# Performance work log

Hardware: AMD Instinct MI355X
Metric: run time of the kernel (lower is better)

## Reference

```python
import jax, jax.numpy as jnp
import numpy as np

B, L, D = 4, 4096, 768
K, Kq, NREP, H, M = 12, 6, 2, 64, 1
KSZ = 4
DIM_MEM = K * H                 # 768
DIM_MEMT = DIM_MEM + K          # 780
DIM_Q = Kq * H * M * 2          # 768
DIM_CONV = DIM_MEMT + DIM_Q     # 1548
DIM_SKIP = D // 4               # 192
DIM_SWH = H * 3 * 2             # 384 (dim_swiglu_head)
DIM_SW = K * DIM_SWH            # 4608
DIM_TOTAL = DIM_CONV + DIM_SKIP + K  # 1752
FLAT = K * H * M                # 768


def _rms(x, w, eps=1e-6):
    return x * jax.lax.rsqrt(jnp.mean(x * x, axis=-1, keepdims=True) + eps) * w


def _dwconv_causal(x, w):
    # depthwise causal conv: x (B,L,C), w (KSZ,C); left-pad KSZ-1
    pad = jnp.pad(x, ((0, 0), (KSZ - 1, 0), (0, 0)))
    Lx = x.shape[1]
    return sum(pad[:, j:j + Lx, :] * w[j] for j in range(KSZ))


def _forward(x, W_in, conv_w, wk, wq, theta_raw, w_int_raw, dt_scale, dt_bias,
             log_A, phase_scale, W_gate, gn_weight, W_readout, W_skip, W_out):
    Bx, Lx, _ = x.shape
    z_all = x @ W_in
    z_conv = z_all[..., :DIM_CONV]
    c_skip = z_all[..., DIM_CONV:DIM_CONV + DIM_SKIP]
    gate_logits = z_all[..., DIM_CONV + DIM_SKIP:]
    z_conv = jax.nn.silu(_dwconv_causal(z_conv, conv_w))
    z_mem = z_conv[..., :DIM_MEMT]
    q_raw = z_conv[..., DIM_MEMT:]
    k_val = _rms(z_mem[..., :DIM_MEM].reshape(Bx, Lx, K, H), wk)
    s_raw = z_mem[..., DIM_MEM:]                       # (B,L,K)
    q = _rms(q_raw, wq).reshape(Bx, Lx, Kq, 1, H, M, 2)
    q_re, q_im = q[..., 0], q[..., 1]
    # M==1 path: theta from logit-parameterized grid, w_int = exp(clipped raw)
    theta = 0.001 + (3.0 - 0.001) * jax.nn.sigmoid(theta_raw)   # (1,1,K,H,1)
    w_int = jnp.exp(jnp.clip(w_int_raw, -5.0, 5.0))             # (1,1,Kq,NREP,H,1)
    dt = jnp.clip(jax.nn.softplus(jnp.clip(dt_scale * s_raw + dt_bias, -20.0, 20.0)), 0.001, 0.1)
    A_disc = jnp.clip(-jnp.exp(log_A) * dt, -20.0, 0.0)         # (B,L,K)
    kf = k_val[..., None]                                       # (B,L,K,H,1)
    ks = kf * phase_scale[None, None, :, None, None]
    phi = ks / (1.0 + jnp.abs(ks)) * theta
    kvw = kf * dt[..., None, None]
    re = kvw * jnp.cos(phi)
    im = kvw * jnp.sin(phi)
    stack = jnp.concatenate([re.reshape(Bx, Lx, FLAT), im.reshape(Bx, Lx, FLAT)], axis=-1)
    decay = jnp.repeat(jnp.exp(A_disc), H * M, axis=-1)
    decay = jnp.concatenate([decay, decay], axis=-1)            # (B,L,2*FLAT)

    def step(carry, inp):
        xt, dc = inp
        s = dc * carry + xt
        return s, s

    init = jnp.zeros((Bx, 2 * FLAT), stack.dtype)
    _, acc = jax.lax.scan(step, init, (stack.transpose(1, 0, 2), decay.transpose(1, 0, 2)))
    acc = acc.transpose(1, 0, 2)                                # (B,L,2*FLAT)
    re_acc = acc[..., :FLAT].reshape(Bx, Lx, Kq, NREP, H, M)
    im_acc = acc[..., FLAT:].reshape(Bx, Lx, Kq, NREP, H, M)
    match_re = re_acc * q_re + im_acc * q_im
    match_im = im_acc * q_re - re_acc * q_im
    out_re = jnp.sum(match_re * w_int, axis=-1).reshape(Bx, Lx, K, H)
    out_im = jnp.sum(match_im * w_int, axis=-1).reshape(Bx, Lx, K, H)
    oc = jnp.concatenate([out_re, out_im], axis=-1).reshape(Bx, Lx, K * 2 * H)
    # GatedRMSNorm: x*sigmoid(gate) -> rmsnorm -> *weight
    g = oc * jax.nn.sigmoid(gate_logits @ W_gate)
    oc_n = _rms(g, gn_weight)
    y_spec = jnp.einsum('blkf,kfn->blkn', oc_n.reshape(Bx, Lx, K, 2 * H), W_readout)
    y_skip = (c_skip @ W_skip).reshape(Bx, Lx, K, DIM_SWH)
    val, gate2 = jnp.split(y_spec + y_skip, 2, axis=-1)
    y = val * jax.nn.silu(gate2)                                # (B,L,K,3H)
    return y.reshape(Bx, Lx, -1) @ W_out                        # (B,L,D)


def setup_inputs() -> dict:
    key = jax.random.key(0)
    ks = jax.random.split(key, 8)
    # theta_raw init: logit of normalized geomspace grid (M==1 branch)
    grid = np.geomspace(0.001, 3.0, K).reshape(1, 1, K, 1, 1)
    base = np.tile(grid, (1, 1, 1, H, 1))
    u = np.clip((base - 0.001) / (3.0 - 0.001), 1e-4, 1 - 1e-4)
    theta_raw = jnp.asarray(np.log(u) - np.log(1 - u), jnp.float32)
    return {
        'x': jax.random.normal(ks[0], (B, L, D), jnp.float32),
        'W_in': jax.random.normal(ks[1], (D, DIM_TOTAL), jnp.float32) * 0.02,
        'conv_w': jax.random.normal(ks[2], (KSZ, DIM_CONV), jnp.float32) * 0.2,
        'wk': jnp.ones((H,), jnp.float32),
        'wq': jnp.ones((DIM_Q,), jnp.float32),
        'theta_raw': theta_raw,
        'w_int_raw': jnp.zeros((1, 1, Kq, NREP, H, M), jnp.float32),
        'dt_scale': jnp.ones((K,), jnp.float32),
        'dt_bias': jnp.asarray(np.log(np.expm1(np.geomspace(0.001, 0.1, K))), jnp.float32),
        'log_A': jnp.asarray(np.log(np.geomspace(1.0, 16.0, K)), jnp.float32),
        'phase_scale': jnp.ones((K,), jnp.float32),
        'W_gate': jax.random.normal(ks[3], (K, K * 2 * H), jnp.float32) * 0.1,
        'gn_weight': jnp.ones((K * 2 * H,), jnp.float32),
        'W_readout': jax.random.normal(ks[4], (K, 2 * H, DIM_SWH), jnp.float32) * float(np.sqrt(2.0 / (2 * H + DIM_SWH))),
        'W_skip': jax.random.normal(ks[5], (DIM_SKIP, DIM_SW), jnp.float32) * 0.02,
        'W_out': jax.random.normal(ks[6], (K * 3 * H, D), jnp.float32) * 0.02,
    }


def reference(x, W_in, conv_w, wk, wq, theta_raw, w_int_raw, dt_scale, dt_bias,
              log_A, phase_scale, W_gate, gn_weight, W_readout, W_skip, W_out):
    return _forward(x, W_in, conv_w, wk, wq, theta_raw, w_int_raw, dt_scale, dt_bias,
                    log_A, phase_scale, W_gate, gn_weight, W_readout, W_skip, W_out)
```

## Files before the change

kernel.cpp:

```cpp
#include <hip/hip_runtime.h>
#include <hip/hip_bf16.h>
#include <cstdint>
#include <cstddef>

#define BB 4
#define LL 4096
#define DD 768
#define KK 12
#define HH 64
#define KSZ 4
#define DIM_MEM 768
#define DIM_MEMT 780
#define DIM_Q 768
#define DIM_CONV 1548
#define DIM_SKIP 192
#define DIM_SWH 384
#define DIM_TOTAL 1752
#define TTOK (BB*LL)
#define NCHUNK 128
#define LCHUNK 32
#define N1REAL 1752
#define N1PAD 1792
#define DGATE (KK*2*HH)

typedef unsigned short ushort_t;
typedef __attribute__((ext_vector_type(8))) short short8v;
typedef __attribute__((ext_vector_type(4))) float f32x4;

__device__ __forceinline__ float sigm(float x) {
    return __builtin_amdgcn_rcpf(1.0f + __expf(-x));
}
__device__ __forceinline__ float softplus_fast(float x) {
    return (x > 0.f) ? (x + __logf(1.0f + __expf(-x))) : __logf(1.0f + __expf(x));
}
__device__ __forceinline__ ushort_t f2bf(float f) {
    __hip_bfloat16 h = __float2bfloat16(f);
    return __builtin_bit_cast(ushort_t, h);
}
__device__ __forceinline__ float bf2f(ushort_t u) {
    const uint32_t i = ((uint32_t)u) << 16;
    return __builtin_bit_cast(float, i);
}
__device__ __forceinline__ float blockReduceSum256(float v, float* sbuf) {
    #pragma unroll
    for (int off = 32; off > 0; off >>= 1) v += __shfl_xor(v, off);
    const int wid = threadIdx.x >> 6;
    __syncthreads();
    if ((threadIdx.x & 63) == 0) sbuf[wid] = v;
    __syncthreads();
    return sbuf[0] + sbuf[1] + sbuf[2] + sbuf[3];
}
__device__ __forceinline__ void gload_lds16(const void* g, void* l) {
    __builtin_amdgcn_global_load_lds(
        (const __attribute__((address_space(1))) void*)g,
        (__attribute__((address_space(3))) void*)l, 16, 0, 0);
}

__launch_bounds__(256)
__global__ void cast_bf16(const float* __restrict__ in, ushort_t* __restrict__ out, int n4) {
    const int stride = gridDim.x * 256;
    for (int i = blockIdx.x * 256 + threadIdx.x; i < n4; i += stride) {
        const float4 v = reinterpret_cast<const float4*>(in)[i];
        ushort4 o;
        o.x = f2bf(v.x); o.y = f2bf(v.y); o.z = f2bf(v.z); o.w = f2bf(v.w);
        reinterpret_cast<ushort4*>(out)[i] = o;
    }
}

__global__ void transpose_cast(const float* __restrict__ in, ushort_t* __restrict__ out,
                               int R, int Cc, int Cpad) {
    __shared__ float tile[32][33];
    const int tx = threadIdx.x, ty = threadIdx.y;
    const int c0 = blockIdx.x * 32, r0 = blockIdx.y * 32;
    #pragma unroll
    for (int rr = ty; rr < 32; rr += 8) {
        const int r = r0 + rr, c = c0 + tx;
        tile[rr][tx] = (r < R && c < Cc) ? in[(size_t)r * Cc + c] : 0.f;
    }
    __syncthreads();
    #pragma unroll
    for (int rr = ty; rr < 32; rr += 8) {
        const int c = c0 + rr, r = r0 + tx;
        if (c < Cpad && r < R)
            out[(size_t)c * R + r] = f2bf(tile[tx][rr]);
    }
}

__global__ void prep_bt(const float* __restrict__ Wr, const float* __restrict__ Wskip,
                        ushort_t* __restrict__ Btv, ushort_t* __restrict__ Btg) {
    const int k = blockIdx.x, n = blockIdx.y, kk = threadIdx.x;
    float v, g;
    if (kk < 128) {
        const size_t base = ((size_t)k * 128 + kk) * DIM_SWH;
        v = Wr[base + n];
        g = Wr[base + 192 + n];
    } else {
        const size_t base = (size_t)(kk - 128) * (KK * DIM_SWH) + (size_t)k * DIM_SWH;
        v = Wskip[base + n];
        g = Wskip[base + 192 + n];
    }
    const size_t o = ((size_t)k * 192 + n) * 320 + kk;
    Btv[o] = f2bf(v);
    Btg[o] = f2bf(g);
}

__global__ void prep_wint(const float* __restrict__ w_int_raw, float* __restrict__ wint) {
    const int i = blockIdx.x * 256 + threadIdx.x;
    if (i < KK * HH) {
        float wr = w_int_raw[i];
        wr = fminf(fmaxf(wr, -5.f), 5.f);
        wint[i] = expf(wr);
    }
}

template <bool BF16OUT>
__launch_bounds__(256)
__global__ void mfma_gemm(const ushort_t* __restrict__ A, const ushort_t* __restrict__ Bt,
                          void* __restrict__ Cv, int Nreal, int K) {
    __shared__ ushort_t As[2][128 * 32];
    __shared__ ushort_t Bs[2][128 * 32];
    const int tid = threadIdx.x;
    const int lane = tid & 63, w = tid >> 6;
    const int m0 = blockIdx.x * 128, n0 = blockIdx.y * 128;
    const int wm = w & 1, wn = w >> 1;
    const int nkt = K >> 5;
    const int lrow = lane >> 2;
    const int lcol = (lane & 3) * 8;

    f32x4 acc[4][4] = {};

    auto stage = [&](int buf, int k0) {
        #pragma unroll
        for (int i = 0; i < 2; ++i) {
            const int seg = w * 2 + i;
            const int row = seg * 16 + lrow;
            gload_lds16(&A[(size_t)(m0 + row) * K + k0 + lcol], &As[buf][seg * 512]);
            gload_lds16(&Bt[(size_t)(n0 + row) * K + k0 + lcol], &Bs[buf][seg * 512]);
        }
    };

    stage(0, 0);
    for (int kt = 0; kt < nkt; ++kt) {
        const int cur = kt & 1;
        __syncthreads();
        if (kt + 1 < nkt) stage(cur ^ 1, (kt + 1) << 5);
        short8v a[4], b[4];
        #pragma unroll
        for (int i = 0; i < 4; ++i)
            a[i] = *(const short8v*)&As[cur][(wm * 64 + i * 16 + (lane & 15)) * 32 + (lane >> 4) * 8];
        #pragma unroll
        for (int j = 0; j < 4; ++j)
            b[j] = *(const short8v*)&Bs[cur][(wn * 64 + j * 16 + (lane & 15)) * 32 + (lane >> 4) * 8];
        #pragma unroll
        for (int i = 0; i < 4; ++i)
            #pragma unroll
            for (int j = 0; j < 4; ++j)
                acc[i][j] = __builtin_amdgcn_mfma_f32_16x16x32_bf16(a[i], b[j], acc[i][j], 0, 0, 0);
    }
    #pragma unroll
    for (int i = 0; i < 4; ++i) {
        const int rbase = m0 + wm * 64 + i * 16 + (lane >> 4) * 4;
        #pragma unroll
        for (int j = 0; j < 4; ++j) {
            const int col = n0 + wn * 64 + j * 16 + (lane & 15);
            if (col < Nreal) {
                #pragma unroll
                for (int r = 0; r < 4; ++r) {
                    if constexpr (BF16OUT)
                        ((ushort_t*)Cv)[(size_t)(rbase + r) * Nreal + col] = f2bf(acc[i][j][r]);
                    else
                        ((float*)Cv)[(size_t)(rbase + r) * Nreal + col] = acc[i][j][r];
                }
            }
        }
    }
}

__launch_bounds__(256)
__global__ void gemm2_mfma(const ushort_t* __restrict__ OCNb, const ushort_t* __restrict__ CskB,
                           const ushort_t* __restrict__ Btv, const ushort_t* __restrict__ Btg,
                           ushort_t* __restrict__ Y) {
    __shared__ ushort_t As[2][128 * 64];
    __shared__ ushort_t Bvs[2][64 * 64];
    __shared__ ushort_t Bgs[2][64 * 64];
    const int tid = threadIdx.x;
    const int lane = tid & 63, w = tid >> 6;
    const int m0 = blockIdx.x * 128;
    const int n0 = blockIdx.y * 64;
    const int k  = blockIdx.z;
    const int wm = w & 1, wn = w >> 1;
    const int lrow = lane >> 3;
    const int lcol = (lane & 7) * 8;
    const ushort_t* btv = Btv + (size_t)k * 192 * 320;
    const ushort_t* btg = Btg + (size_t)k * 192 * 320;

    f32x4 accV[4][2] = {};
    f32x4 accG[4][2] = {};

    auto stage = [&](int buf, int kt) {
        #pragma unroll
        for (int i = 0; i < 4; ++i) {
            const int seg = w * 4 + i;
            const int row = seg * 8 + lrow;
            const ushort_t* src = (kt < 2)
                ? OCNb + (size_t)(m0 + row) * DGATE + k * 128 + kt * 64 + lcol
                : CskB + (size_t)(m0 + row) * DIM_SKIP + (kt - 2) * 64 + lcol;
            gload_lds16(src, &As[buf][seg * 512]);
        }
        #pragma unroll
        for (int i = 0; i < 2; ++i) {
            const int seg = w * 2 + i;
            const int row = seg * 8 + lrow;
            gload_lds16(btv + (size_t)(n0 + row) * 320 + kt * 64 + lcol, &Bvs[buf][seg * 512]);
            gload_lds16(btg + (size_t)(n0 + row) * 320 + kt * 64 + lcol, &Bgs[buf][seg * 512]);
        }
    };

    stage(0, 0);
    for (int kt = 0; kt < 5; ++kt) {
        const int cur = kt & 1;
        __syncthreads();
        if (kt + 1 < 5) stage(cur ^ 1, kt + 1);
        #pragma unroll
        for (int kk = 0; kk < 2; ++kk) {
            short8v a[4], bv[2], bg[2];
            #pragma unroll
            for (int i = 0; i < 4; ++i)
                a[i] = *(const short8v*)&As[cur][(wm * 64 + i * 16 + (lane & 15)) * 64 + kk * 32 + (lane >> 4) * 8];
            #pragma unroll
            for (int j = 0; j < 2; ++j) {
                bv[j] = *(const short8v*)&Bvs[cur][(wn * 32 + j * 16 + (lane & 15)) * 64 + kk * 32 + (lane >> 4) * 8];
                bg[j] = *(const short8v*)&Bgs[cur][(wn * 32 + j * 16 + (lane & 15)) * 64 + kk * 32 + (lane >> 4) * 8];
            }
            #pragma unroll
            for (int i = 0; i < 4; ++i)
                #pragma unroll
                for (int j = 0; j < 2; ++j) {
                    accV[i][j] = __builtin_amdgcn_mfma_f32_16x16x32_bf16(a[i], bv[j], accV[i][j], 0, 0, 0);
                    accG[i][j] = __builtin_amdgcn_mfma_f32_16x16x32_bf16(a[i], bg[j], accG[i][j], 0, 0, 0);
                }
        }
    }
    #pragma unroll
    for (int i = 0; i < 4; ++i) {
        const int rbase = m0 + wm * 64 + i * 16 + (lane >> 4) * 4;
        #pragma unroll
        for (int j = 0; j < 2; ++j) {
            const int col = k * 192 + n0 + wn * 32 + j * 16 + (lane & 15);
            #pragma unroll
            for (int r = 0; r < 4; ++r) {
                const float g = accG[i][j][r];
                Y[(size_t)(rbase + r) * (KK * 3 * HH) + col] = f2bf(accV[i][j][r] * (g * sigm(g)));
            }
        }
    }
}

__launch_bounds__(64)
__global__ void feat_scan(const ushort_t* __restrict__ Zb, const float* __restrict__ conv_w,
                          const float* __restrict__ wk, const float* __restrict__ theta_raw,
                          const float* __restrict__ dt_scale, const float* __restrict__ dt_bias,
                          const float* __restrict__ log_A, const float* __restrict__ phase_scale,
                          float2* __restrict__ acc, float* __restrict__ pcum,
                          float2* __restrict__ cend, float* __restrict__ cp) {
    const int blk = blockIdx.x;
    const int bk = blk / NCHUNK, chunk = blk - bk * NCHUNK;
    const int b = bk / KK, k = bk - b * KK;
    const int h = threadIdx.x;
    const int t0 = chunk * LCHUNK;
    const int cm_ch = k * HH + h;
    const int cs_ch = DIM_MEM + k;

    const float w0 = conv_w[0 * DIM_CONV + cm_ch];
    const float w1 = conv_w[1 * DIM_CONV + cm_ch];
    const float w2 = conv_w[2 * DIM_CONV + cm_ch];
    const float w3 = conv_w[3 * DIM_CONV + cm_ch];
    const float s0 = conv_w[0 * DIM_CONV + cs_ch];
    const float s1 = conv_w[1 * DIM_CONV + cs_ch];
    const float s2 = conv_w[2 * DIM_CONV + cs_ch];
    const float s3 = conv_w[3 * DIM_CONV + cs_ch];
    const float wkh = wk[h];
    const float th = 0.001f + (3.0f - 0.001f) * sigm(theta_raw[cm_ch]);
    const float ps = phase_scale[k];
    const float dts = dt_scale[k], dtb = dt_bias[k];
    const float eA = expf(log_A[k]);

    const size_t rowb = (size_t)b * LL;
    auto zm_at = [&](int t) -> float {
        return (t >= 0) ? bf2f(Zb[(rowb + t) * DIM_TOTAL + cm_ch]) : 0.f;
    };
    auto zs_at = [&](int t) -> float {
        return (t >= 0) ? bf2f(Zb[(rowb + t) * DIM_TOTAL + cs_ch]) : 0.f;
    };
    float zm3 = zm_at(t0 - 3), zm2 = zm_at(t0 - 2), zm1 = zm_at(t0 - 1);
    float zs3 = zs_at(t0 - 3), zs2 = zs_at(t0 - 2), zs1 = zs_at(t0 - 1);

    float are = 0.f, aim = 0.f, P = 1.f;
    #pragma unroll 4
    for (int tt = 0; tt < LCHUNK; ++tt) {
        const int t = t0 + tt;
        const float zm0 = bf2f(Zb[(rowb + t) * DIM_TOTAL + cm_ch]);
        const float zs0 = bf2f(Zb[(rowb + t) * DIM_TOTAL + cs_ch]);
        float cm = fmaf(w0, zm3, fmaf(w1, zm2, fmaf(w2, zm1, w3 * zm0)));
        float cs = fmaf(s0, zs3, fmaf(s1, zs2, fmaf(s2, zs1, s3 * zs0)));
        const float um = cm * sigm(cm);
        const float us = cs * sigm(cs);
        float ssq = um * um;
        #pragma unroll
        for (int off = 32; off > 0; off >>= 1) ssq += __shfl_xor(ssq, off);
        const float kval = um * rsqrtf(ssq * (1.0f / (float)HH) + 1e-6f) * wkh;
        float lin = fminf(fmaxf(fmaf(dts, us, dtb), -20.f), 20.f);
        float dt = fminf(fmaxf(softplus_fast(lin), 0.001f), 0.1f);
        const float Ad = fminf(fmaxf(-eA * dt, -20.f), 0.f);
        const float dec = __expf(Ad);
        const float ks = kval * ps;
        const float phi = ks / (1.0f + fabsf(ks)) * th;
        const float kvw = kval * dt;
        float sp, cq;
        __sincosf(phi, &sp, &cq);
        are = fmaf(dec, are, kvw * cq);
        aim = fmaf(dec, aim, kvw * sp);
        P *= dec;
        acc[((size_t)bk * LL + t) * HH + h] = make_float2(are, aim);
        if (h == 0) pcum[(size_t)bk * LL + t] = P;
        zm3 = zm2; zm2 = zm1; zm1 = zm0;
        zs3 = zs2; zs2 = zs1; zs1 = zs0;
    }
    cend[(size_t)blk * HH + h] = make_float2(are, aim);
    if (h == 0) cp[blk] = P;
}

__launch_bounds__(128)
__global__ void scan_b(const float* __restrict__ cend, const float* __restrict__ cp,
                       float* __restrict__ carry) {
    const int bk = blockIdx.x;
    const int c = threadIdx.x;
    float cur = 0.f;
    for (int ch = 0; ch < NCHUNK; ++ch) {
        const size_t idx = (size_t)bk * NCHUNK + ch;
        carry[idx * 128 + c] = cur;
        cur = fmaf(cp[idx], cur, cend[idx * 128 + c]);
    }
}

__launch_bounds__(256)
__global__ void combine_kernel(const float2* __restrict__ acc, const float* __restrict__ pcum,
                               const float2* __restrict__ carry, const ushort_t* __restrict__ Zb,
                               const float* __restrict__ conv_w, const float* __restrict__ wq,
                               const float* __restrict__ wintG, const float* __restrict__ W_gate,
                               const float* __restrict__ gn_weight,
                               ushort_t* __restrict__ ocnB, ushort_t* __restrict__ cskB) {
    __shared__ float q_sh[DIM_Q];
    __shared__ float g_sh[DGATE];
    __shared__ float gl[KK];
    __shared__ float red[8];
    const int tok = blockIdx.x;
    const int b = tok / LL, t = tok % LL;
    const int tid = threadIdx.x;
    const int chunk = t / LCHUNK;
    const size_t zrow = (size_t)tok * DIM_TOTAL;

    if (tid < KK) gl[tid] = bf2f(Zb[zrow + DIM_CONV + DIM_SKIP + tid]);
    if (tid < DIM_SKIP) cskB[(size_t)tok * DIM_SKIP + tid] = Zb[zrow + DIM_CONV + tid];

    float part = 0.f;
    float qv[3];
    #pragma unroll
    for (int it = 0; it < 3; ++it) {
        const int c = tid + it * 256;
        const int ch = DIM_MEMT + c;
        float s = 0.f;
        #pragma unroll
        for (int j = 0; j < KSZ; ++j) {
            const int tt2 = t + j - (KSZ - 1);
            if (tt2 >= 0)
                s = fmaf(conv_w[j * DIM_CONV + ch],
                         bf2f(Zb[((size_t)(b * LL + tt2)) * DIM_TOTAL + ch]), s);
        }
        const float u = s * sigm(s);
        qv[it] = u;
        part = fmaf(u, u, part);
    }
    const float qss = blockReduceSum256(part, red);
    const float qrs = rsqrtf(qss / (float)DIM_Q + 1e-6f);
    #pragma unroll
    for (int it = 0; it < 3; ++it) {
        const int c = tid + it * 256;
        q_sh[c] = qv[it] * qrs * wq[c];
    }
    __syncthreads();

    float part2 = 0.f;
    #pragma unroll
    for (int it = 0; it < 3; ++it) {
        const int p = tid + it * 256;
        const int k = p >> 6, h = p & 63;
        const int kq = k >> 1;
        const size_t bkL = (size_t)(b * KK + k) * LL + t;
        const float pc = pcum[bkL];
        const float2 a2 = acc[bkL * HH + h];
        const float2 c2 = carry[((size_t)(b * KK + k) * NCHUNK + chunk) * HH + h];
        const float re = fmaf(pc, c2.x, a2.x);
        const float im = fmaf(pc, c2.y, a2.y);
        const float qre = q_sh[kq * 128 + 2 * h];
        const float qim = q_sh[kq * 128 + 2 * h + 1];
        const float wint = wintG[p];
        const float ore = (re * qre + im * qim) * wint;
        const float oim = (im * qre - re * qim) * wint;
        float gr = 0.f, gi = 0.f;
        const int cre = k * 128 + h, cim = k * 128 + 64 + h;
        #pragma unroll
        for (int i = 0; i < KK; ++i) {
            gr = fmaf(gl[i], W_gate[i * DGATE + cre], gr);
            gi = fmaf(gl[i], W_gate[i * DGATE + cim], gi);
        }
        const float g_re = ore * sigm(gr);
        const float g_im = oim * sigm(gi);
        g_sh[cre] = g_re;
        g_sh[cim] = g_im;
        part2 = fmaf(g_re, g_re, part2);
        part2 = fmaf(g_im, g_im, part2);
    }
    const float ss = blockReduceSum256(part2, red);
    const float rs = rsqrtf(ss / (float)DGATE + 1e-6f);
    __syncthreads();
    #pragma unroll
    for (int it = 0; it < 6; ++it) {
        const int c = tid + it * 256;
        ocnB[(size_t)tok * DGATE + c] = f2bf(g_sh[c] * rs * gn_weight[c]);
    }
}

static inline size_t pass_need_bytes(int TP) {
    const size_t BP = (size_t)TP / LL;
    size_t total = 0;
    total += (size_t)TP * DIM_TOTAL * 2;
    total += (size_t)TP * KK * HH * 8;
    total += (size_t)TP * KK * 4;
    total += BP * KK * NCHUNK * HH * 8;
    total += BP * KK * NCHUNK * 4;
    total += BP * KK * NCHUNK * HH * 8;
    total += (size_t)TP * (DGATE + DIM_SKIP) * 2;
    total += 8ull * 1024 * 1024;
    return total;
}

extern "C" void kernel_launch(void* const* d_in, const int* in_sizes, int n_in,
                              void* d_out, int out_size, void* d_ws, size_t ws_size,
                              hipStream_t stream) {
    const float* x           = (const float*)d_in[0];
    const float* W_in        = (const float*)d_in[1];
    const float* conv_w      = (const float*)d_in[2];
    const float* wk          = (const float*)d_in[3];
    const float* wq          = (const float*)d_in[4];
    const float* theta_raw   = (const float*)d_in[5];
    const float* w_int_raw   = (const float*)d_in[6];
    const float* dt_scale    = (const float*)d_in[7];
    const float* dt_bias     = (const float*)d_in[8];
    const float* log_A       = (const float*)d_in[9];
    const float* phase_scale = (const float*)d_in[10];
    const float* W_gate      = (const float*)d_in[11];
    const float* gn_weight   = (const float*)d_in[12];
    const float* W_readout   = (const float*)d_in[13];
    const float* W_skip      = (const float*)d_in[14];
    const float* W_out       = (const float*)d_in[15];
    float* out = (float*)d_out;

    int passes = 4;
    if (ws_size >= pass_need_bytes(TTOK))        passes = 1;
    else if (ws_size >= pass_need_bytes(TTOK/2)) passes = 2;

    const int BP = BB / passes;
    const int TP = BP * LL;

    char* p = (char*)d_ws;
    ushort_t* Zb   = (ushort_t*)p;               p += (size_t)TP * DIM_TOTAL * 2;
    char* accR     = p;
    float2* acc    = (float2*)p;                 p += (size_t)TP * KK * HH * 8;
    float* pcum    = (float*)p;                  p += (size_t)TP * KK * 4;
    float2* cendv  = (float2*)p;                 p += (size_t)BP * KK * NCHUNK * HH * 8;
    float* cp      = (float*)p;                  p += (size_t)BP * KK * NCHUNK * 4;
    float2* carry  = (float2*)p;                 p += (size_t)BP * KK * NCHUNK * HH * 8;
    char* ocnR     = p;
    ushort_t* ocnB = (ushort_t*)p;               p += (size_t)TP * DGATE * 2;
    ushort_t* cskB = (ushort_t*)p;               p += (size_t)TP * DIM_SKIP * 2;
    ushort_t* WoutT= (ushort_t*)p;               p += (size_t)768 * 2304 * 2;
    ushort_t* Btv  = (ushort_t*)p;               p += (size_t)KK * 192 * 320 * 2;
    ushort_t* Btg  = (ushort_t*)p;               p += (size_t)KK * 192 * 320 * 2;
    float* wintG   = (float*)p;                  p += (size_t)KK * HH * 4;
    ushort_t* xb   = (ushort_t*)ocnR;
    ushort_t* WinT = (ushort_t*)accR;
    ushort_t* Y    = (ushort_t*)accR;

    for (int pass = 0; pass < passes; ++pass) {
        const float* xp = x   + (size_t)pass * TP * DD;
        float*       op = out + (size_t)pass * TP * DD;

        cast_bf16<<<1024, 256, 0, stream>>>(xp, xb, TP * DD / 4);
        transpose_cast<<<dim3(N1PAD / 32, DD / 32), dim3(32, 8), 0, stream>>>(
            W_in, WinT, DD, N1REAL, N1PAD);
        transpose_cast<<<dim3(DD / 32, (KK * 3 * HH) / 32), dim3(32, 8), 0, stream>>>(
            W_out, WoutT, KK * 3 * HH, DD, DD);
        prep_bt<<<dim3(KK, 192), 320, 0, stream>>>(W_readout, W_skip, Btv, Btg);
        prep_wint<<<3, 256, 0, stream>>>(w_int_raw, wintG);

        mfma_gemm<true><<<dim3(TP / 128, N1PAD / 128), 256, 0, stream>>>(xb, WinT, Zb, N1REAL, DD);

        feat_scan<<<BP * KK * NCHUNK, 64, 0, stream>>>(Zb, conv_w, wk, theta_raw, dt_scale,
                                                       dt_bias, log_A, phase_scale,
                                                       acc, pcum, cendv, cp);

        scan_b<<<BP * KK, 128, 0, stream>>>((const float*)cendv, cp, (float*)carry);

        combine_kernel<<<TP, 256, 0, stream>>>(acc, pcum, carry, Zb, conv_w, wq, wintG,
                                               W_gate, gn_weight, ocnB, cskB);

        gemm2_mfma<<<dim3(TP / 128, 3, KK), 256, 0, stream>>>(ocnB, cskB, Btv, Btg, Y);

        mfma_gemm<false><<<dim3(TP / 128, DD / 128), 256, 0, stream>>>(Y, WoutT, op, DD, KK * 3 * HH);
    }
}
```

Baseline: 407.9 us.

## Process one token per wavefront in combine kernel, replacing block reductions

The combine step now gives each 64-lane wavefront its own token, with four tokens per 256-thread block. Both RMS reductions become wave shuffles, so the block-wide __syncthreads barriers and shared reduction buffers go away. Gate values stay in registers instead of a shared staging array, and the skip-channel copy uses vectorized 4-element loads. The cost is higher register pressure per lane (12-element arrays) and a 4x smaller grid.

```diff
diff --git a/kernel.cpp b/kernel.cpp
--- a/kernel.cpp
+++ b/kernel.cpp
@@ -41,14 +41,10 @@
     const uint32_t i = ((uint32_t)u) << 16;
     return __builtin_bit_cast(float, i);
 }
-__device__ __forceinline__ float blockReduceSum256(float v, float* sbuf) {
+__device__ __forceinline__ float waveReduceSum(float v) {
     #pragma unroll
     for (int off = 32; off > 0; off >>= 1) v += __shfl_xor(v, off);
-    const int wid = threadIdx.x >> 6;
-    __syncthreads();
-    if ((threadIdx.x & 63) == 0) sbuf[wid] = v;
-    __syncthreads();
-    return sbuf[0] + sbuf[1] + sbuf[2] + sbuf[3];
+    return v;
 }
 __device__ __forceinline__ void gload_lds16(const void* g, void* l) {
     __builtin_amdgcn_global_load_lds(
@@ -344,30 +340,33 @@
 }
 
 __launch_bounds__(256)
-__global__ void combine_kernel(const float2* __restrict__ acc, const float* __restrict__ pcum,
-                               const float2* __restrict__ carry, const ushort_t* __restrict__ Zb,
-                               const float* __restrict__ conv_w, const float* __restrict__ wq,
-                               const float* __restrict__ wintG, const float* __restrict__ W_gate,
-                               const float* __restrict__ gn_weight,
-                               ushort_t* __restrict__ ocnB, ushort_t* __restrict__ cskB) {
-    __shared__ float q_sh[DIM_Q];
-    __shared__ float g_sh[DGATE];
-    __shared__ float gl[KK];
-    __shared__ float red[8];
-    const int tok = blockIdx.x;
+__global__ void combine_wave(const float2* __restrict__ acc, const float* __restrict__ pcum,
+                             const float2* __restrict__ carry, const ushort_t* __restrict__ Zb,
+                             const float* __restrict__ conv_w, const float* __restrict__ wq,
+                             const float* __restrict__ wintG, const float* __restrict__ W_gate,
+                             const float* __restrict__ gn_weight,
+                             ushort_t* __restrict__ ocnB, ushort_t* __restrict__ cskB) {
+    __shared__ float q_sh[4][DIM_Q];
+    const int w = threadIdx.x >> 6, lane = threadIdx.x & 63;
+    const int tok = blockIdx.x * 4 + w;
     const int b = tok / LL, t = tok % LL;
-    const int tid = threadIdx.x;
     const int chunk = t / LCHUNK;
     const size_t zrow = (size_t)tok * DIM_TOTAL;
 
-    if (tid < KK) gl[tid] = bf2f(Zb[zrow + DIM_CONV + DIM_SKIP + tid]);
-    if (tid < DIM_SKIP) cskB[(size_t)tok * DIM_SKIP + tid] = Zb[zrow + DIM_CONV + tid];
-
-    float part = 0.f;
-    float qv[3];
-    #pragma unroll
-    for (int it = 0; it < 3; ++it) {
-        const int c = tid + it * 256;
+    if (lane < 48) {
+        const ushort4 v = *reinterpret_cast<const ushort4*>(&Zb[zrow + DIM_CONV + lane * 4]);
+        *reinterpret_cast<ushort4*>(&cskB[(size_t)tok * DIM_SKIP + lane * 4]) = v;
+    }
+
+    float gl[KK];
+    #pragma unroll
+    for (int i = 0; i < KK; ++i) gl[i] = bf2f(Zb[zrow + DIM_CONV + DIM_SKIP + i]);
+
+    float u[12];
+    float ssq = 0.f;
+    #pragma unroll
+    for (int i = 0; i < 12; ++i) {
+        const int c = i * 64 + lane;
         const int ch = DIM_MEMT + c;
         float s = 0.f;
         #pragma unroll
@@ -377,57 +376,52 @@
                 s = fmaf(conv_w[j * DIM_CONV + ch],
                          bf2f(Zb[((size_t)(b * LL + tt2)) * DIM_TOTAL + ch]), s);
         }
-        const float u = s * sigm(s);
-        qv[it] = u;
-        part = fmaf(u, u, part);
-    }
-    const float qss = blockReduceSum256(part, red);
-    const float qrs = rsqrtf(qss / (float)DIM_Q + 1e-6f);
-    #pragma unroll
-    for (int it = 0; it < 3; ++it) {
-        const int c = tid + it * 256;
-        q_sh[c] = qv[it] * qrs * wq[c];
-    }
-    __syncthreads();
-
+        const float uu = s * sigm(s);
+        u[i] = uu;
+        ssq = fmaf(uu, uu, ssq);
+    }
+    ssq = waveReduceSum(ssq);
+    const float qrs = rsqrtf(ssq * (1.0f / (float)DIM_Q) + 1e-6f);
+    #pragma unroll
+    for (int i = 0; i < 12; ++i) {
+        const int c = i * 64 + lane;
+        q_sh[w][c] = u[i] * qrs * wq[c];
+    }
+
+    float gre[KK], gim[KK];
     float part2 = 0.f;
-    #pragma unroll
-    for (int it = 0; it < 3; ++it) {
-        const int p = tid + it * 256;
-        const int k = p >> 6, h = p & 63;
-        const int kq = k >> 1;
+    float2 q2 = make_float2(0.f, 0.f);
+    #pragma unroll
+    for (int k = 0; k < KK; ++k) {
+        if ((k & 1) == 0)
+            q2 = *reinterpret_cast<const float2*>(&q_sh[w][(k >> 1) * 128 + 2 * lane]);
         const size_t bkL = (size_t)(b * KK + k) * LL + t;
         const float pc = pcum[bkL];
-        const float2 a2 = acc[bkL * HH + h];
-        const float2 c2 = carry[((size_t)(b * KK + k) * NCHUNK + chunk) * HH + h];
+        const float2 a2 = acc[bkL * HH + lane];
+        const float2 c2 = carry[((size_t)(b * KK + k) * NCHUNK + chunk) * HH + lane];
         const float re = fmaf(pc, c2.x, a2.x);
         const float im = fmaf(pc, c2.y, a2.y);
-        const float qre = q_sh[kq * 128 + 2 * h];
-        const float qim = q_sh[kq * 128 + 2 * h + 1];
-        const float wint = wintG[p];
-        const float ore = (re * qre + im * qim) * wint;
-        const float oim = (im * qre - re * qim) * wint;
+        const float wint = wintG[k * HH + lane];
+        const float ore = (re * q2.x + im * q2.y) * wint;
+        const float oim = (im * q2.x - re * q2.y) * wint;
         float gr = 0.f, gi = 0.f;
-        const int cre = k * 128 + h, cim = k * 128 + 64 + h;
         #pragma unroll
         for (int i = 0; i < KK; ++i) {
-            gr = fmaf(gl[i], W_gate[i * DGATE + cre], gr);
-            gi = fmaf(gl[i], W_gate[i * DGATE + cim], gi);
-        }
-        const float g_re = ore * sigm(gr);
-        const float g_im = oim * sigm(gi);
-        g_sh[cre] = g_re;
-        g_sh[cim] = g_im;
-        part2 = fmaf(g_re, g_re, part2);
-        part2 = fmaf(g_im, g_im, part2);
-    }
-    const float ss = blockReduceSum256(part2, red);
-    const float rs = rsqrtf(ss / (float)DGATE + 1e-6f);
-    __syncthreads();
-    #pragma unroll
-    for (int it = 0; it < 6; ++it) {
-        const int c = tid + it * 256;
-        ocnB[(size_t)tok * DGATE + c] = f2bf(g_sh[c] * rs * gn_weight[c]);
+            gr = fmaf(gl[i], W_gate[i * DGATE + k * 128 + lane], gr);
+            gi = fmaf(gl[i], W_gate[i * DGATE + k * 128 + 64 + lane], gi);
+        }
+        gre[k] = ore * sigm(gr);
+        gim[k] = oim * sigm(gi);
+        part2 = fmaf(gre[k], gre[k], part2);
+        part2 = fmaf(gim[k], gim[k], part2);
+    }
+    part2 = waveReduceSum(part2);
+    const float rs = rsqrtf(part2 * (1.0f / (float)DGATE) + 1e-6f);
+    #pragma unroll
+    for (int k = 0; k < KK; ++k) {
+        const int cre = k * 128 + lane, cim = k * 128 + 64 + lane;
+        ocnB[(size_t)tok * DGATE + cre] = f2bf(gre[k] * rs * gn_weight[cre]);
+        ocnB[(size_t)tok * DGATE + cim] = f2bf(gim[k] * rs * gn_weight[cim]);
     }
 }
 
@@ -512,8 +506,8 @@
 
         scan_b<<<BP * KK, 128, 0, stream>>>((const float*)cendv, cp, (float*)carry);
 
-        combine_kernel<<<TP, 256, 0, stream>>>(acc, pcum, carry, Zb, conv_w, wq, wintG,
-                                               W_gate, gn_weight, ocnB, cskB);
+        combine_wave<<<TP / 4, 256, 0, stream>>>(acc, pcum, carry, Zb, conv_w, wq, wintG,
+                                                 W_gate, gn_weight, ocnB, cskB);
 
         gemm2_mfma<<<dim3(TP / 128, 3, KK), 256, 0, stream>>>(ocnB, cskB, Btv, Btg, Y);
 
```

Result: slower. 442.0 us (+8.4%).
